# Performance work log

Hardware: AMD Instinct MI355X
Metric: run time of the kernel (lower is better)

Reference implementation:

```python
import jax, jax.numpy as jnp
import numpy as np

N = 50000
E = 800000
IN_CH = 128
HID = 64
HEADS = 4
EPS = 1e-5
NEG_SLOPE = 0.2


def _gat_conv(x, src, dst, W, a_src, a_dst, b, heads, out_ch, concat):
    n = x.shape[0]
    h = (x @ W).reshape(n, heads, out_ch)                      # [N,H,C]
    alpha_src = jnp.sum(h * a_src, axis=-1)                    # [N,H]
    alpha_dst = jnp.sum(h * a_dst, axis=-1)                    # [N,H]
    e = jax.nn.leaky_relu(alpha_src[src] + alpha_dst[dst], NEG_SLOPE)  # [E',H]
    # segment softmax over incoming edges of each destination node
    m = jax.ops.segment_max(e, dst, num_segments=n)            # [N,H]
    e = jnp.exp(e - m[dst])
    denom = jax.ops.segment_sum(e, dst, num_segments=n)        # [N,H]
    alpha = e / denom[dst]                                     # [E',H]
    msg = h[src] * alpha[:, :, None]                           # [E',H,C]
    out = jax.ops.segment_sum(msg, dst, num_segments=n)        # [N,H,C]
    if concat:
        out = out.reshape(n, heads * out_ch)
    else:
        out = out.mean(axis=1)
    return out + b


def _bn_eval(x, gamma, beta, mean, var):
    return (x - mean) * (gamma / jnp.sqrt(var + EPS)) + beta


def setup_inputs() -> dict:
    key = jax.random.key(0)
    ks = jax.random.split(key, 24)
    s = 0.1
    x = jax.random.normal(ks[0], (N, IN_CH), dtype=jnp.float32)
    edge_index = jax.random.randint(ks[1], (2, E), 0, N, dtype=jnp.int32)
    d0, d1 = IN_CH, HID * HEADS
    inp = {
        'x': x, 'edge_index': edge_index,
        # layer 0: in_ch -> hidden, heads=4, concat
        'W0': jax.random.normal(ks[2], (d0, HEADS * HID), jnp.float32) * s,
        'as0': jax.random.normal(ks[3], (HEADS, HID), jnp.float32) * s,
        'ad0': jax.random.normal(ks[4], (HEADS, HID), jnp.float32) * s,
        'b0': jax.random.normal(ks[5], (HEADS * HID,), jnp.float32) * s,
        # layer 1: hidden*heads -> hidden, heads=4, concat
        'W1': jax.random.normal(ks[6], (d1, HEADS * HID), jnp.float32) * s,
        'as1': jax.random.normal(ks[7], (HEADS, HID), jnp.float32) * s,
        'ad1': jax.random.normal(ks[8], (HEADS, HID), jnp.float32) * s,
        'b1': jax.random.normal(ks[9], (HEADS * HID,), jnp.float32) * s,
        # layer 2: hidden*heads -> 1, heads=1, no concat
        'W2': jax.random.normal(ks[10], (d1, 1), jnp.float32) * s,
        'as2': jax.random.normal(ks[11], (1, 1), jnp.float32) * s,
        'ad2': jax.random.normal(ks[12], (1, 1), jnp.float32) * s,
        'b2': jax.random.normal(ks[13], (1,), jnp.float32) * s,
        # batchnorm (eval) params for the two hidden layers
        'g0': jnp.ones((d1,), jnp.float32),
        'be0': jnp.zeros((d1,), jnp.float32),
        'm0': jax.random.normal(ks[14], (d1,), jnp.float32) * s,
        'v0': jnp.ones((d1,), jnp.float32),
        'g1': jnp.ones((d1,), jnp.float32),
        'be1': jnp.zeros((d1,), jnp.float32),
        'm1': jax.random.normal(ks[15], (d1,), jnp.float32) * s,
        'v1': jnp.ones((d1,), jnp.float32),
    }
    return inp


def reference(x, edge_index, W0, as0, ad0, b0, W1, as1, ad1, b1,
              W2, as2, ad2, b2, g0, be0, m0, v0, g1, be1, m1, v1):
    n = x.shape[0]
    loops = jnp.arange(n, dtype=edge_index.dtype)
    src = jnp.concatenate([edge_index[0], loops])  # add self-loops (PyG default)
    dst = jnp.concatenate([edge_index[1], loops])

    # layer 0 (no residual: shapes differ)
    h = _gat_conv(x, src, dst, W0, as0, ad0, b0, HEADS, HID, True)
    h = jax.nn.elu(_bn_eval(h, g0, be0, m0, v0))

    # layer 1 (residual: shapes match)
    res = h
    h = _gat_conv(h, src, dst, W1, as1, ad1, b1, HEADS, HID, True)
    h = jax.nn.elu(_bn_eval(h, g1, be1, m1, v1)) + res

    # output layer: heads=1, concat=False -> [N,1]
    out = _gat_conv(h, src, dst, W2, as2, ad2, b2, 1, 1, False)
    return out.squeeze(-1)
```

## Files before the change

kernel.cpp:

```cpp
#include <hip/hip_runtime.h>
#include <math.h>

#define NEG_SLOPE 0.2f
#define BN_EPS 1e-5f

typedef __attribute__((ext_vector_type(8))) short bf16x8;
typedef __attribute__((ext_vector_type(4))) float f32x4;

static __device__ __forceinline__ unsigned short f2bf(float f){
    unsigned u = __float_as_uint(f);
    u += 0x7FFFu + ((u >> 16) & 1u);
    return (unsigned short)(u >> 16);
}
static __device__ __forceinline__ float bf2f(unsigned short v){
    return __uint_as_float((unsigned)v << 16);
}

static __device__ __forceinline__ void gload_lds16(const void* g, void* l){
    __builtin_amdgcn_global_load_lds(
        (const __attribute__((address_space(1))) void*)g,
        (__attribute__((address_space(3))) void*)l, 16, 0, 0);
}

__global__ void conv_hilo_kernel(const float* __restrict__ x,
                                 unsigned short* __restrict__ hi,
                                 unsigned short* __restrict__ lo, int n4)
{
    int i = blockIdx.x * 256 + threadIdx.x;
    if (i >= n4) return;
    const float4 v = ((const float4*)x)[i];
    ushort4 h4, l4;
    h4.x = f2bf(v.x); l4.x = f2bf(v.x - bf2f(h4.x));
    h4.y = f2bf(v.y); l4.y = f2bf(v.y - bf2f(h4.y));
    h4.z = f2bf(v.z); l4.z = f2bf(v.z - bf2f(h4.z));
    h4.w = f2bf(v.w); l4.w = f2bf(v.w - bf2f(h4.w));
    ((ushort4*)hi)[i] = h4; ((ushort4*)lo)[i] = l4;
}

__global__ void repack_w_kernel(const float* __restrict__ W,
                                unsigned short* __restrict__ wbhi,
                                unsigned short* __restrict__ wblo)
{
    const int o = blockIdx.x * 256 + threadIdx.x;
    const int j = o & 7, ln = (o >> 3) & 63, ct = (o >> 9) & 15, kt = o >> 13;
    const int k = kt * 32 + 8 * (ln >> 4) + j;
    const int col = ct * 16 + (ln & 15);
    const float v = W[k * 256 + col];
    const unsigned short hb = f2bf(v);
    wbhi[o] = hb; wblo[o] = f2bf(v - bf2f(hb));
}

template<int K>
__global__ __launch_bounds__(256) void mfma_gemm_alpha(
    const unsigned short* __restrict__ xhi, const unsigned short* __restrict__ xlo,
    const unsigned short* __restrict__ wbhi, const unsigned short* __restrict__ wblo,
    const float* __restrict__ a_s, const float* __restrict__ a_d,
    unsigned short* __restrict__ hout,
    float* __restrict__ asrc, float* __restrict__ adst, int N)
{
    __shared__ unsigned short xa[8][512];
    __shared__ unsigned short wb[32][512];
    const int t = threadIdx.x, lane = t & 63, wid = t >> 6;
    const int n0 = blockIdx.x * 64;

    f32x4 acc[4][4];
#pragma unroll
    for (int rt = 0; rt < 4; ++rt)
#pragma unroll
        for (int q = 0; q < 4; ++q) acc[rt][q] = (f32x4){0.f, 0.f, 0.f, 0.f};

    for (int kt = 0; kt < K / 32; ++kt){
        __syncthreads();
#pragma unroll
        for (int ii = 0; ii < 2; ++ii){
            const int i = wid * 2 + ii;
            const int rt = i >> 1, plane = i & 1;
            int node = n0 + rt * 16 + (lane & 15);
            if (node > N - 1) node = N - 1;
            const unsigned short* src = (plane ? xlo : xhi)
                + (size_t)node * K + kt * 32 + 8 * (lane >> 4);
            gload_lds16(src, &xa[i][0]);
        }
#pragma unroll
        for (int ii = 0; ii < 8; ++ii){
            const int i = wid * 8 + ii;
            const int ct = i >> 1, plane = i & 1;
            const unsigned short* base = plane ? wblo : wbhi;
            gload_lds16(base + ((size_t)(kt * 16 + ct) * 64 + lane) * 8, &wb[i][0]);
        }
        __syncthreads();

        bf16x8 a[4][2];
#pragma unroll
        for (int rt = 0; rt < 4; ++rt)
#pragma unroll
            for (int pl = 0; pl < 2; ++pl)
                a[rt][pl] = *(const bf16x8*)&xa[rt * 2 + pl][lane * 8];

#pragma unroll
        for (int q = 0; q < 4; ++q){
            const int cti = wid * 4 + q;
            const bf16x8 bhi = *(const bf16x8*)&wb[cti * 2 + 0][lane * 8];
            const bf16x8 blo = *(const bf16x8*)&wb[cti * 2 + 1][lane * 8];
#pragma unroll
            for (int rt = 0; rt < 4; ++rt){
                acc[rt][q] = __builtin_amdgcn_mfma_f32_16x16x32_bf16(a[rt][0], bhi, acc[rt][q], 0, 0, 0);
                acc[rt][q] = __builtin_amdgcn_mfma_f32_16x16x32_bf16(a[rt][1], bhi, acc[rt][q], 0, 0, 0);
                acc[rt][q] = __builtin_amdgcn_mfma_f32_16x16x32_bf16(a[rt][0], blo, acc[rt][q], 0, 0, 0);
            }
        }
    }

    const int l15 = lane & 15, lg = lane >> 4;
    float avs[4], avd[4];
#pragma unroll
    for (int q = 0; q < 4; ++q){
        avs[q] = a_s[wid * 64 + q * 16 + l15];
        avd[q] = a_d[wid * 64 + q * 16 + l15];
    }
    float sp[4][4], dp[4][4];
#pragma unroll
    for (int rt = 0; rt < 4; ++rt){
#pragma unroll
        for (int reg = 0; reg < 4; ++reg){
            const int node = n0 + rt * 16 + lg * 4 + reg;
            float s = 0.f, d = 0.f;
            unsigned short hv[4];
#pragma unroll
            for (int q = 0; q < 4; ++q){
                const float v = acc[rt][q][reg];
                s = fmaf(v, avs[q], s); d = fmaf(v, avd[q], d);
                hv[q] = f2bf(v);
            }
            if (node < N){
#pragma unroll
                for (int q = 0; q < 4; ++q)
                    hout[(size_t)node * 256 + (wid * 4 + q) * 16 + l15] = hv[q];
            }
            sp[rt][reg] = s; dp[rt][reg] = d;
        }
    }
#pragma unroll
    for (int off = 1; off <= 8; off <<= 1){
#pragma unroll
        for (int rt = 0; rt < 4; ++rt)
#pragma unroll
            for (int reg = 0; reg < 4; ++reg){
                sp[rt][reg] += __shfl_xor(sp[rt][reg], off, 64);
                dp[rt][reg] += __shfl_xor(dp[rt][reg], off, 64);
            }
    }
    if (l15 == 0){
#pragma unroll
        for (int rt = 0; rt < 4; ++rt)
#pragma unroll
            for (int reg = 0; reg < 4; ++reg){
                const int node = n0 + rt * 16 + lg * 4 + reg;
                if (node < N){
                    asrc[(size_t)node * 4 + wid] = sp[rt][reg];
                    adst[(size_t)node * 4 + wid] = dp[rt][reg];
                }
            }
    }
}

__global__ void deg_init_kernel(int* __restrict__ deg, int N){
    int i = blockIdx.x * blockDim.x + threadIdx.x;
    if (i < N) deg[i] = 1;
}

__global__ void deg_hist_kernel(const int* __restrict__ ei, int E, int* __restrict__ deg){
    int e = blockIdx.x * blockDim.x + threadIdx.x;
    if (e < E) atomicAdd(&deg[ei[E + e]], 1);
}

__global__ __launch_bounds__(256) void part_sum_kernel(const int* __restrict__ deg,
                                                       int* __restrict__ bsum, int N)
{
    __shared__ int red[256];
    const int t = threadIdx.x;
    const int i0 = blockIdx.x * 1024 + t * 4;
    int s = 0;
    if (i0 + 3 < N){
        const int4 v = *(const int4*)&deg[i0];
        s = v.x + v.y + v.z + v.w;
    } else {
#pragma unroll
        for (int j = 0; j < 4; ++j) if (i0 + j < N) s += deg[i0 + j];
    }
    red[t] = s; __syncthreads();
    for (int off = 128; off >= 1; off >>= 1){
        if (t < off) red[t] += red[t + off];
        __syncthreads();
    }
    if (t == 0) bsum[blockIdx.x] = red[0];
}

__global__ __launch_bounds__(256) void scan_part_kernel(int* __restrict__ bsum, int nb,
                                                        int* __restrict__ row, int N)
{
    __shared__ int sh[256];
    const int t = threadIdx.x;
    const int v = (t < nb) ? bsum[t] : 0;
    sh[t] = v; __syncthreads();
    for (int off = 1; off < 256; off <<= 1){
        int u = (t >= off) ? sh[t - off] : 0;
        __syncthreads();
        sh[t] += u;
        __syncthreads();
    }
    if (t < nb) bsum[t] = sh[t] - v;
    if (t == nb - 1) row[N] = sh[t];
}

__global__ __launch_bounds__(256) void distribute_kernel(const int* __restrict__ deg,
    const int* __restrict__ bsum, int* __restrict__ row, int* __restrict__ cursor, int N)
{
    __shared__ int ts[256];
    const int t = threadIdx.x;
    const int i0 = blockIdx.x * 1024 + t * 4;
    int d[4]; int s = 0;
#pragma unroll
    for (int j = 0; j < 4; ++j){ d[j] = (i0 + j < N) ? deg[i0 + j] : 0; s += d[j]; }
    ts[t] = s; __syncthreads();
    for (int off = 1; off < 256; off <<= 1){
        int u = (t >= off) ? ts[t - off] : 0;
        __syncthreads();
        ts[t] += u;
        __syncthreads();
    }
    int base = bsum[blockIdx.x] + ts[t] - s;
#pragma unroll
    for (int j = 0; j < 4; ++j){
        if (i0 + j < N){ row[i0 + j] = base; cursor[i0 + j] = base; base += d[j]; }
    }
}

__global__ void scatter_kernel(const int* __restrict__ ei, int E, int N,
                               int* __restrict__ cursor, int* __restrict__ csr)
{
    int e = blockIdx.x * blockDim.x + threadIdx.x;
    if (e >= E + N) return;
    int s, d;
    if (e < E){ s = ei[e]; d = ei[E + e]; } else { s = d = e - E; }
    int pos = atomicAdd(&cursor[d], 1);
    csr[pos] = s;
}

#define DEG_CAP 128
__global__ __launch_bounds__(256) void agg4_kernel(
    const int* __restrict__ row, const int* __restrict__ csr,
    const float* __restrict__ asrc, const float* __restrict__ adst,
    const unsigned short* __restrict__ h,
    const float* __restrict__ b, const float* __restrict__ g,
    const float* __restrict__ be, const float* __restrict__ mean,
    const float* __restrict__ var,
    const unsigned short* __restrict__ reshi, const unsigned short* __restrict__ reslo,
    unsigned short* __restrict__ outhi, unsigned short* __restrict__ outlo, int N)
{
    __shared__ float plds[4][(DEG_CAP + 4) * 4];
    __shared__ int   slds[4][DEG_CAP + 4];
    const int wid = threadIdx.x >> 6, lane = threadIdx.x & 63;
    const int node = blockIdx.x * 4 + wid;
    if (node >= N) return;
    const int beg = row[node], end = row[node + 1], deg = end - beg;
    const int degc = deg < DEG_CAP ? deg : DEG_CAP;
    const int head = lane >> 4;

    const float4 ad = *(const float4*)&adst[(size_t)node * 4];

    float d0 = 0.f, d1 = 0.f, d2 = 0.f, d3 = 0.f;
    for (int i = lane; i < deg; i += 64){
        const int s = csr[beg + i];
        const float4 as = *(const float4*)&asrc[(size_t)s * 4];
        float v0 = as.x + ad.x, v1 = as.y + ad.y, v2 = as.z + ad.z, v3 = as.w + ad.w;
        v0 = v0 > 0.f ? v0 : NEG_SLOPE * v0;
        v1 = v1 > 0.f ? v1 : NEG_SLOPE * v1;
        v2 = v2 > 0.f ? v2 : NEG_SLOPE * v2;
        v3 = v3 > 0.f ? v3 : NEG_SLOPE * v3;
        const float p0 = __expf(v0), p1 = __expf(v1);
        const float p2 = __expf(v2), p3 = __expf(v3);
        d0 += p0; d1 += p1; d2 += p2; d3 += p3;
        if (i < DEG_CAP){
            *(float4*)&plds[wid][i * 4] = make_float4(p0, p1, p2, p3);
            slds[wid][i] = s << 9;
        }
    }
    if (lane < 4){
        const int slot = degc + lane;
        *(float4*)&plds[wid][slot * 4] = make_float4(0.f, 0.f, 0.f, 0.f);
        slds[wid][slot] = 0;
    }
    for (int off = 32; off >= 1; off >>= 1){
        d0 += __shfl_xor(d0, off, 64); d1 += __shfl_xor(d1, off, 64);
        d2 += __shfl_xor(d2, off, 64); d3 += __shfl_xor(d3, off, 64);
    }

    float a0 = 0.f, a1 = 0.f, a2 = 0.f, a3 = 0.f;
    {
        const char* hb = (const char*)h + lane * 8;
        const float* pb = &plds[wid][0];
        const int* sb = &slds[wid][0];
        ushort4 hA = *(const ushort4*)(hb + sb[0]);
        ushort4 hB = *(const ushort4*)(hb + sb[1]);
        for (int i = 0; i < degc; i += 2){
            const ushort4 hC = *(const ushort4*)(hb + sb[i + 2]);
            const ushort4 hD = *(const ushort4*)(hb + sb[i + 3]);
            const float pA = pb[i * 4 + head];
            const float pB = pb[(i + 1) * 4 + head];
            a0 = fmaf(pA, bf2f(hA.x), a0); a1 = fmaf(pA, bf2f(hA.y), a1);
            a2 = fmaf(pA, bf2f(hA.z), a2); a3 = fmaf(pA, bf2f(hA.w), a3);
            a0 = fmaf(pB, bf2f(hB.x), a0); a1 = fmaf(pB, bf2f(hB.y), a1);
            a2 = fmaf(pB, bf2f(hB.z), a2); a3 = fmaf(pB, bf2f(hB.w), a3);
            hA = hC; hB = hD;
        }
    }

    for (int jj = beg + DEG_CAP; jj < end; ++jj){
        const int s = csr[jj];
        const float4 as = *(const float4*)&asrc[(size_t)s * 4];
        float e0 = as.x + ad.x, e1 = as.y + ad.y, e2 = as.z + ad.z, e3 = as.w + ad.w;
        float eh = (head == 0) ? e0 : (head == 1) ? e1 : (head == 2) ? e2 : e3;
        eh = eh > 0.f ? eh : NEG_SLOPE * eh;
        const float p = __expf(eh);
        const ushort4 hv = *(const ushort4*)&h[(size_t)s * 256 + lane * 4];
        a0 = fmaf(p, bf2f(hv.x), a0); a1 = fmaf(p, bf2f(hv.y), a1);
        a2 = fmaf(p, bf2f(hv.z), a2); a3 = fmaf(p, bf2f(hv.w), a3);
    }

    const int l15 = lane & 15;
    const float dsel = (head == 0) ? d0 : (head == 1) ? d1 : (head == 2) ? d2 : d3;
    const float rdi = 1.f / dsel;
    const int c0 = head * 64 + 4 * l15;
    const float4 bv  = *(const float4*)&b[c0];
    const float4 gv  = *(const float4*)&g[c0];
    const float4 bev = *(const float4*)&be[c0];
    const float4 mv  = *(const float4*)&mean[c0];
    const float4 vv4 = *(const float4*)&var[c0];
    const float ava[4]  = {a0, a1, a2, a3};
    const float bva[4]  = {bv.x, bv.y, bv.z, bv.w};
    const float gva[4]  = {gv.x, gv.y, gv.z, gv.w};
    const float beva[4] = {bev.x, bev.y, bev.z, bev.w};
    const float mva[4]  = {mv.x, mv.y, mv.z, mv.w};
    const float vva[4]  = {vv4.x, vv4.y, vv4.z, vv4.w};
    float rh[4] = {0.f, 0.f, 0.f, 0.f};
    if (reshi){
        const ushort4 r1 = *(const ushort4*)&reshi[(size_t)node * 256 + c0];
        const ushort4 r2 = *(const ushort4*)&reslo[(size_t)node * 256 + c0];
        rh[0] = bf2f(r1.x) + bf2f(r2.x); rh[1] = bf2f(r1.y) + bf2f(r2.y);
        rh[2] = bf2f(r1.z) + bf2f(r2.z); rh[3] = bf2f(r1.w) + bf2f(r2.w);
    }
    unsigned short hos[4], los[4];
#pragma unroll
    for (int j = 0; j < 4; ++j){
        float vvv = ava[j] * rdi + bva[j];
        vvv = (vvv - mva[j]) * (gva[j] * rsqrtf(vva[j] + BN_EPS)) + beva[j];
        vvv = vvv > 0.f ? vvv : (__expf(vvv) - 1.f);
        vvv += rh[j];
        const unsigned short hb2 = f2bf(vvv);
        hos[j] = hb2; los[j] = f2bf(vvv - bf2f(hb2));
    }
    ushort4 ho, lo4;
    ho.x = hos[0];  ho.y = hos[1];  ho.z = hos[2];  ho.w = hos[3];
    lo4.x = los[0]; lo4.y = los[1]; lo4.z = los[2]; lo4.w = los[3];
    *(ushort4*)&outhi[(size_t)node * 256 + c0] = ho;
    *(ushort4*)&outlo[(size_t)node * 256 + c0] = lo4;
}

__global__ __launch_bounds__(256) void gemm2_kernel(
    const unsigned short* __restrict__ xhi, const unsigned short* __restrict__ xlo,
    const float* __restrict__ W2, float* __restrict__ h2, int N)
{
    const int wid = threadIdx.x >> 6, lane = threadIdx.x & 63;
    const int n = blockIdx.x * 4 + wid;
    if (n >= N) return;
    float sum = 0.f;
#pragma unroll
    for (int i = 0; i < 4; ++i){
        const int c = i * 64 + lane;
        sum += (bf2f(xhi[(size_t)n * 256 + c]) + bf2f(xlo[(size_t)n * 256 + c])) * W2[c];
    }
    for (int off = 32; off >= 1; off >>= 1) sum += __shfl_xor(sum, off, 64);
    if (lane == 0) h2[n] = sum;
}

__global__ void agg2_kernel(const int* __restrict__ row, const int* __restrict__ csr,
                            const float* __restrict__ h2,
                            const float* __restrict__ as2, const float* __restrict__ ad2,
                            const float* __restrict__ b2, float* __restrict__ out, int N)
{
    const int n = blockIdx.x * blockDim.x + threadIdx.x;
    if (n >= N) return;
    const float A_s = as2[0];
    const float hd  = h2[n] * ad2[0];
    const int beg = row[n], end = row[n + 1];
    float den = 0.f, acc = 0.f;
    for (int i = beg; i < end; ++i){
        const float hv = h2[csr[i]];
        float a = fmaf(A_s, hv, hd);
        a = a > 0.f ? a : NEG_SLOPE * a;
        const float p = __expf(a);
        den += p; acc = fmaf(p, hv, acc);
    }
    out[n] = acc / den + b2[0];
}

extern "C" void kernel_launch(void* const* d_in, const int* in_sizes, int n_in,
                              void* d_out, int out_size, void* d_ws, size_t ws_size,
                              hipStream_t stream)
{
    const float* x   = (const float*)d_in[0];
    const int*   ei  = (const int*)  d_in[1];
    const float* W0  = (const float*)d_in[2];
    const float* as0 = (const float*)d_in[3];
    const float* ad0 = (const float*)d_in[4];
    const float* b0  = (const float*)d_in[5];
    const float* W1  = (const float*)d_in[6];
    const float* as1 = (const float*)d_in[7];
    const float* ad1 = (const float*)d_in[8];
    const float* b1  = (const float*)d_in[9];
    const float* W2  = (const float*)d_in[10];
    const float* as2 = (const float*)d_in[11];
    const float* ad2 = (const float*)d_in[12];
    const float* b2  = (const float*)d_in[13];
    const float* g0  = (const float*)d_in[14];
    const float* be0 = (const float*)d_in[15];
    const float* m0  = (const float*)d_in[16];
    const float* v0  = (const float*)d_in[17];
    const float* g1  = (const float*)d_in[18];
    const float* be1 = (const float*)d_in[19];
    const float* m1  = (const float*)d_in[20];
    const float* v1  = (const float*)d_in[21];

    const int N = in_sizes[0] / 128;
    const int E = in_sizes[1] / 2;
    const int EN = E + N;

    char* w = (char*)d_ws;
    unsigned short* H    = (unsigned short*)w;  w += (size_t)N * 256 * 2;
    unsigned short* X0hi = (unsigned short*)w;
    unsigned short* X0lo = X0hi + (size_t)N * 128;
    unsigned short* P1hi = X0hi;
    w += (size_t)N * 256 * 2;
    unsigned short* P0hi = (unsigned short*)w;  w += (size_t)N * 256 * 2;
    unsigned short* P0lo = (unsigned short*)w;  w += (size_t)N * 256 * 2;
    unsigned short* P1lo = (unsigned short*)w;  w += (size_t)N * 256 * 2;
    float*    asrc   = (float*)w;   w += (size_t)N * 4 * 4;
    float*    adst   = (float*)w;   w += (size_t)N * 4 * 4;
    int*      deg    = (int*)w;     w += (size_t)N * 4;
    int*      cursor = (int*)w;     w += (size_t)N * 4;
    int*      csr    = (int*)w;     w += (size_t)EN * 4;
    float*    h2     = (float*)w;   w += (size_t)N * 4;
    int*      bsum   = (int*)w;     w += 1024;
    unsigned short* Wb0hi = (unsigned short*)w; w += (size_t)128 * 256 * 2;
    unsigned short* Wb0lo = (unsigned short*)w; w += (size_t)128 * 256 * 2;
    unsigned short* Wb1hi = (unsigned short*)w; w += (size_t)256 * 256 * 2;
    unsigned short* Wb1lo = (unsigned short*)w; w += (size_t)256 * 256 * 2;
    int*      rowp   = (int*)w;     w += (size_t)(N + 1) * 4;

    const int gN64  = (N + 63) / 64;
    const int gN4   = (N + 3) / 4;
    const int gNt   = (N + 255) / 256;
    const int gE    = (E + 255) / 256;
    const int gEN   = (EN + 255) / 256;
    const int nb    = (N + 1023) / 1024;

    conv_hilo_kernel<<<(N * 128 / 4 + 255) / 256, 256, 0, stream>>>(x, X0hi, X0lo, N * 128 / 4);
    repack_w_kernel<<<128, 256, 0, stream>>>(W0, Wb0hi, Wb0lo);
    repack_w_kernel<<<256, 256, 0, stream>>>(W1, Wb1hi, Wb1lo);
    deg_init_kernel<<<gNt, 256, 0, stream>>>(deg, N);
    deg_hist_kernel<<<gE, 256, 0, stream>>>(ei, E, deg);
    part_sum_kernel<<<nb, 256, 0, stream>>>(deg, bsum, N);
    scan_part_kernel<<<1, 256, 0, stream>>>(bsum, nb, rowp, N);
    distribute_kernel<<<nb, 256, 0, stream>>>(deg, bsum, rowp, cursor, N);
    scatter_kernel<<<gEN, 256, 0, stream>>>(ei, E, N, cursor, csr);

    mfma_gemm_alpha<128><<<gN64, 256, 0, stream>>>(X0hi, X0lo, Wb0hi, Wb0lo,
                                                   as0, ad0, H, asrc, adst, N);
    agg4_kernel<<<gN4, 256, 0, stream>>>(rowp, csr, asrc, adst, H,
                                         b0, g0, be0, m0, v0,
                                         nullptr, nullptr, P0hi, P0lo, N);

    mfma_gemm_alpha<256><<<gN64, 256, 0, stream>>>(P0hi, P0lo, Wb1hi, Wb1lo,
                                                   as1, ad1, H, asrc, adst, N);
    agg4_kernel<<<gN4, 256, 0, stream>>>(rowp, csr, asrc, adst, H,
                                         b1, g1, be1, m1, v1,
                                         P0hi, P0lo, P1hi, P1lo, N);

    gemm2_kernel<<<gN4, 256, 0, stream>>>(P1hi, P1lo, W2, h2, N);
    agg2_kernel<<<gNt, 256, 0, stream>>>(rowp, csr, h2, as2, ad2, b2, (float*)d_out, N);
}
```

Baseline: 346.0 us.

## Fuse hi/lo split into GEMM, fold layer-2 GEMV into aggregation, merge prep kernels

```diff
diff --git a/kernel.cpp b/kernel.cpp
--- a/kernel.cpp
+++ b/kernel.cpp
@@ -22,43 +22,43 @@
         (__attribute__((address_space(3))) void*)l, 16, 0, 0);
 }
 
-__global__ void conv_hilo_kernel(const float* __restrict__ x,
-                                 unsigned short* __restrict__ hi,
-                                 unsigned short* __restrict__ lo, int n4)
-{
-    int i = blockIdx.x * 256 + threadIdx.x;
-    if (i >= n4) return;
-    const float4 v = ((const float4*)x)[i];
-    ushort4 h4, l4;
-    h4.x = f2bf(v.x); l4.x = f2bf(v.x - bf2f(h4.x));
-    h4.y = f2bf(v.y); l4.y = f2bf(v.y - bf2f(h4.y));
-    h4.z = f2bf(v.z); l4.z = f2bf(v.z - bf2f(h4.z));
-    h4.w = f2bf(v.w); l4.w = f2bf(v.w - bf2f(h4.w));
-    ((ushort4*)hi)[i] = h4; ((ushort4*)lo)[i] = l4;
-}
-
-__global__ void repack_w_kernel(const float* __restrict__ W,
-                                unsigned short* __restrict__ wbhi,
-                                unsigned short* __restrict__ wblo)
-{
-    const int o = blockIdx.x * 256 + threadIdx.x;
+static __device__ __forceinline__ void repack_one(const float* __restrict__ W,
+    unsigned short* __restrict__ whi, unsigned short* __restrict__ wlo, int o)
+{
     const int j = o & 7, ln = (o >> 3) & 63, ct = (o >> 9) & 15, kt = o >> 13;
     const int k = kt * 32 + 8 * (ln >> 4) + j;
     const int col = ct * 16 + (ln & 15);
     const float v = W[k * 256 + col];
     const unsigned short hb = f2bf(v);
-    wbhi[o] = hb; wblo[o] = f2bf(v - bf2f(hb));
+    whi[o] = hb; wlo[o] = f2bf(v - bf2f(hb));
+}
+
+__global__ void prep_kernel(const float* __restrict__ W0,
+    unsigned short* __restrict__ w0hi, unsigned short* __restrict__ w0lo,
+    const float* __restrict__ W1,
+    unsigned short* __restrict__ w1hi, unsigned short* __restrict__ w1lo,
+    int* __restrict__ deg, int N)
+{
+    const int bid = blockIdx.x, t = threadIdx.x;
+    if (bid < 128){
+        repack_one(W0, w0hi, w0lo, bid * 256 + t);
+    } else if (bid < 384){
+        repack_one(W1, w1hi, w1lo, (bid - 128) * 256 + t);
+    } else {
+        const int i = (bid - 384) * 256 + t;
+        if (i < N) deg[i] = 1;
+    }
 }
 
 template<int K>
 __global__ __launch_bounds__(256) void mfma_gemm_alpha(
-    const unsigned short* __restrict__ xhi, const unsigned short* __restrict__ xlo,
+    const float* __restrict__ x,
     const unsigned short* __restrict__ wbhi, const unsigned short* __restrict__ wblo,
     const float* __restrict__ a_s, const float* __restrict__ a_d,
     unsigned short* __restrict__ hout,
     float* __restrict__ asrc, float* __restrict__ adst, int N)
 {
-    __shared__ unsigned short xa[8][512];
+    __shared__ float xaf[4][2][64][4];
     __shared__ unsigned short wb[32][512];
     const int t = threadIdx.x, lane = t & 63, wid = t >> 6;
     const int n0 = blockIdx.x * 64;
@@ -74,12 +74,11 @@
 #pragma unroll
         for (int ii = 0; ii < 2; ++ii){
             const int i = wid * 2 + ii;
-            const int rt = i >> 1, plane = i & 1;
+            const int rt = i >> 1, half = i & 1;
             int node = n0 + rt * 16 + (lane & 15);
             if (node > N - 1) node = N - 1;
-            const unsigned short* src = (plane ? xlo : xhi)
-                + (size_t)node * K + kt * 32 + 8 * (lane >> 4);
-            gload_lds16(src, &xa[i][0]);
+            const float* src = &x[(size_t)node * K + kt * 32 + 8 * (lane >> 4) + half * 4];
+            gload_lds16(src, &xaf[rt][half][0][0]);
         }
 #pragma unroll
         for (int ii = 0; ii < 8; ++ii){
@@ -90,12 +89,19 @@
         }
         __syncthreads();
 
-        bf16x8 a[4][2];
-#pragma unroll
-        for (int rt = 0; rt < 4; ++rt)
-#pragma unroll
-            for (int pl = 0; pl < 2; ++pl)
-                a[rt][pl] = *(const bf16x8*)&xa[rt * 2 + pl][lane * 8];
+        bf16x8 ahi[4], alo[4];
+#pragma unroll
+        for (int rt = 0; rt < 4; ++rt){
+            const float4 f0 = *(const float4*)&xaf[rt][0][lane][0];
+            const float4 f1 = *(const float4*)&xaf[rt][1][lane][0];
+            const float fv[8] = {f0.x, f0.y, f0.z, f0.w, f1.x, f1.y, f1.z, f1.w};
+#pragma unroll
+            for (int j = 0; j < 8; ++j){
+                const unsigned short hb = f2bf(fv[j]);
+                ahi[rt][j] = (short)hb;
+                alo[rt][j] = (short)f2bf(fv[j] - bf2f(hb));
+            }
+        }
 
 #pragma unroll
         for (int q = 0; q < 4; ++q){
@@ -104,9 +110,9 @@
             const bf16x8 blo = *(const bf16x8*)&wb[cti * 2 + 1][lane * 8];
 #pragma unroll
             for (int rt = 0; rt < 4; ++rt){
-                acc[rt][q] = __builtin_amdgcn_mfma_f32_16x16x32_bf16(a[rt][0], bhi, acc[rt][q], 0, 0, 0);
-                acc[rt][q] = __builtin_amdgcn_mfma_f32_16x16x32_bf16(a[rt][1], bhi, acc[rt][q], 0, 0, 0);
-                acc[rt][q] = __builtin_amdgcn_mfma_f32_16x16x32_bf16(a[rt][0], blo, acc[rt][q], 0, 0, 0);
+                acc[rt][q] = __builtin_amdgcn_mfma_f32_16x16x32_bf16(ahi[rt], bhi, acc[rt][q], 0, 0, 0);
+                acc[rt][q] = __builtin_amdgcn_mfma_f32_16x16x32_bf16(alo[rt], bhi, acc[rt][q], 0, 0, 0);
+                acc[rt][q] = __builtin_amdgcn_mfma_f32_16x16x32_bf16(ahi[rt], blo, acc[rt][q], 0, 0, 0);
             }
         }
     }
@@ -162,11 +168,6 @@
                 }
             }
     }
-}
-
-__global__ void deg_init_kernel(int* __restrict__ deg, int N){
-    int i = blockIdx.x * blockDim.x + threadIdx.x;
-    if (i < N) deg[i] = 1;
 }
 
 __global__ void deg_hist_kernel(const int* __restrict__ ei, int E, int* __restrict__ deg){
@@ -248,6 +249,7 @@
 }
 
 #define DEG_CAP 128
+template<bool LAST>
 __global__ __launch_bounds__(256) void agg4_kernel(
     const int* __restrict__ row, const int* __restrict__ csr,
     const float* __restrict__ asrc, const float* __restrict__ adst,
@@ -255,11 +257,13 @@
     const float* __restrict__ b, const float* __restrict__ g,
     const float* __restrict__ be, const float* __restrict__ mean,
     const float* __restrict__ var,
-    const unsigned short* __restrict__ reshi, const unsigned short* __restrict__ reslo,
-    unsigned short* __restrict__ outhi, unsigned short* __restrict__ outlo, int N)
-{
-    __shared__ float plds[4][(DEG_CAP + 4) * 4];
-    __shared__ int   slds[4][DEG_CAP + 4];
+    const float* __restrict__ res,
+    float* __restrict__ outp,
+    const float* __restrict__ W2,
+    int N)
+{
+    __shared__ float plds[4][DEG_CAP * 4];
+    __shared__ int   slds[4][DEG_CAP];
     const int wid = threadIdx.x >> 6, lane = threadIdx.x & 63;
     const int node = blockIdx.x * 4 + wid;
     if (node >= N) return;
@@ -286,11 +290,6 @@
             slds[wid][i] = s << 9;
         }
     }
-    if (lane < 4){
-        const int slot = degc + lane;
-        *(float4*)&plds[wid][slot * 4] = make_float4(0.f, 0.f, 0.f, 0.f);
-        slds[wid][slot] = 0;
-    }
     for (int off = 32; off >= 1; off >>= 1){
         d0 += __shfl_xor(d0, off, 64); d1 += __shfl_xor(d1, off, 64);
         d2 += __shfl_xor(d2, off, 64); d3 += __shfl_xor(d3, off, 64);
@@ -301,19 +300,20 @@
         const char* hb = (const char*)h + lane * 8;
         const float* pb = &plds[wid][0];
         const int* sb = &slds[wid][0];
-        ushort4 hA = *(const ushort4*)(hb + sb[0]);
-        ushort4 hB = *(const ushort4*)(hb + sb[1]);
-        for (int i = 0; i < degc; i += 2){
-            const ushort4 hC = *(const ushort4*)(hb + sb[i + 2]);
-            const ushort4 hD = *(const ushort4*)(hb + sb[i + 3]);
-            const float pA = pb[i * 4 + head];
-            const float pB = pb[(i + 1) * 4 + head];
-            a0 = fmaf(pA, bf2f(hA.x), a0); a1 = fmaf(pA, bf2f(hA.y), a1);
-            a2 = fmaf(pA, bf2f(hA.z), a2); a3 = fmaf(pA, bf2f(hA.w), a3);
-            a0 = fmaf(pB, bf2f(hB.x), a0); a1 = fmaf(pB, bf2f(hB.y), a1);
-            a2 = fmaf(pB, bf2f(hB.z), a2); a3 = fmaf(pB, bf2f(hB.w), a3);
-            hA = hC; hB = hD;
-        }
+#define EDGE_BODY(slot)                                                        \
+        {                                                                      \
+            const float p_ = pb[(slot) * 4 + head];                            \
+            const ushort4 hv_ = *(const ushort4*)(hb + sb[slot]);              \
+            a0 = fmaf(p_, bf2f(hv_.x), a0); a1 = fmaf(p_, bf2f(hv_.y), a1);    \
+            a2 = fmaf(p_, bf2f(hv_.z), a2); a3 = fmaf(p_, bf2f(hv_.w), a3);    \
+        }
+        int i = 0;
+        for (; i + 2 <= degc; i += 2){
+            EDGE_BODY(i);
+            EDGE_BODY(i + 1);
+        }
+        for (; i < degc; ++i) EDGE_BODY(i);
+#undef EDGE_BODY
     }
 
     for (int jj = beg + DEG_CAP; jj < end; ++jj){
@@ -344,44 +344,27 @@
     const float mva[4]  = {mv.x, mv.y, mv.z, mv.w};
     const float vva[4]  = {vv4.x, vv4.y, vv4.z, vv4.w};
     float rh[4] = {0.f, 0.f, 0.f, 0.f};
-    if (reshi){
-        const ushort4 r1 = *(const ushort4*)&reshi[(size_t)node * 256 + c0];
-        const ushort4 r2 = *(const ushort4*)&reslo[(size_t)node * 256 + c0];
-        rh[0] = bf2f(r1.x) + bf2f(r2.x); rh[1] = bf2f(r1.y) + bf2f(r2.y);
-        rh[2] = bf2f(r1.z) + bf2f(r2.z); rh[3] = bf2f(r1.w) + bf2f(r2.w);
-    }
-    unsigned short hos[4], los[4];
+    if (LAST){
+        const float4 rv = *(const float4*)&res[(size_t)node * 256 + c0];
+        rh[0] = rv.x; rh[1] = rv.y; rh[2] = rv.z; rh[3] = rv.w;
+    }
+    float vvv[4];
 #pragma unroll
     for (int j = 0; j < 4; ++j){
-        float vvv = ava[j] * rdi + bva[j];
-        vvv = (vvv - mva[j]) * (gva[j] * rsqrtf(vva[j] + BN_EPS)) + beva[j];
-        vvv = vvv > 0.f ? vvv : (__expf(vvv) - 1.f);
-        vvv += rh[j];
-        const unsigned short hb2 = f2bf(vvv);
-        hos[j] = hb2; los[j] = f2bf(vvv - bf2f(hb2));
-    }
-    ushort4 ho, lo4;
-    ho.x = hos[0];  ho.y = hos[1];  ho.z = hos[2];  ho.w = hos[3];
-    lo4.x = los[0]; lo4.y = los[1]; lo4.z = los[2]; lo4.w = los[3];
-    *(ushort4*)&outhi[(size_t)node * 256 + c0] = ho;
-    *(ushort4*)&outlo[(size_t)node * 256 + c0] = lo4;
-}
-
-__global__ __launch_bounds__(256) void gemm2_kernel(
-    const unsigned short* __restrict__ xhi, const unsigned short* __restrict__ xlo,
-    const float* __restrict__ W2, float* __restrict__ h2, int N)
-{
-    const int wid = threadIdx.x >> 6, lane = threadIdx.x & 63;
-    const int n = blockIdx.x * 4 + wid;
-    if (n >= N) return;
-    float sum = 0.f;
-#pragma unroll
-    for (int i = 0; i < 4; ++i){
-        const int c = i * 64 + lane;
-        sum += (bf2f(xhi[(size_t)n * 256 + c]) + bf2f(xlo[(size_t)n * 256 + c])) * W2[c];
-    }
-    for (int off = 32; off >= 1; off >>= 1) sum += __shfl_xor(sum, off, 64);
-    if (lane == 0) h2[n] = sum;
+        float v = ava[j] * rdi + bva[j];
+        v = (v - mva[j]) * (gva[j] * rsqrtf(vva[j] + BN_EPS)) + beva[j];
+        v = v > 0.f ? v : (__expf(v) - 1.f);
+        vvv[j] = v + rh[j];
+    }
+    if (!LAST){
+        *(float4*)&outp[(size_t)node * 256 + c0] =
+            make_float4(vvv[0], vvv[1], vvv[2], vvv[3]);
+    } else {
+        const float4 w2v = *(const float4*)&W2[c0];
+        float part = vvv[0] * w2v.x + vvv[1] * w2v.y + vvv[2] * w2v.z + vvv[3] * w2v.w;
+        for (int off = 32; off >= 1; off >>= 1) part += __shfl_xor(part, off, 64);
+        if (lane == 0) outp[node] = part;
+    }
 }
 
 __global__ void agg2_kernel(const int* __restrict__ row, const int* __restrict__ csr,
@@ -437,14 +420,8 @@
     const int EN = E + N;
 
     char* w = (char*)d_ws;
-    unsigned short* H    = (unsigned short*)w;  w += (size_t)N * 256 * 2;
-    unsigned short* X0hi = (unsigned short*)w;
-    unsigned short* X0lo = X0hi + (size_t)N * 128;
-    unsigned short* P1hi = X0hi;
-    w += (size_t)N * 256 * 2;
-    unsigned short* P0hi = (unsigned short*)w;  w += (size_t)N * 256 * 2;
-    unsigned short* P0lo = (unsigned short*)w;  w += (size_t)N * 256 * 2;
-    unsigned short* P1lo = (unsigned short*)w;  w += (size_t)N * 256 * 2;
+    unsigned short* H  = (unsigned short*)w;  w += (size_t)N * 256 * 2;
+    float*    P0     = (float*)w;   w += (size_t)N * 256 * 4;
     float*    asrc   = (float*)w;   w += (size_t)N * 4 * 4;
     float*    adst   = (float*)w;   w += (size_t)N * 4 * 4;
     int*      deg    = (int*)w;     w += (size_t)N * 4;
@@ -465,28 +442,24 @@
     const int gEN   = (EN + 255) / 256;
     const int nb    = (N + 1023) / 1024;
 
-    conv_hilo_kernel<<<(N * 128 / 4 + 255) / 256, 256, 0, stream>>>(x, X0hi, X0lo, N * 128 / 4);
-    repack_w_kernel<<<128, 256, 0, stream>>>(W0, Wb0hi, Wb0lo);
-    repack_w_kernel<<<256, 256, 0, stream>>>(W1, Wb1hi, Wb1lo);
-    deg_init_kernel<<<gNt, 256, 0, stream>>>(deg, N);
+    prep_kernel<<<384 + gNt, 256, 0, stream>>>(W0, Wb0hi, Wb0lo, W1, Wb1hi, Wb1lo, deg, N);
     deg_hist_kernel<<<gE, 256, 0, stream>>>(ei, E, deg);
     part_sum_kernel<<<nb, 256, 0, stream>>>(deg, bsum, N);
     scan_part_kernel<<<1, 256, 0, stream>>>(bsum, nb, rowp, N);
     distribute_kernel<<<nb, 256, 0, stream>>>(deg, bsum, rowp, cursor, N);
     scatter_kernel<<<gEN, 256, 0, stream>>>(ei, E, N, cursor, csr);
 
-    mfma_gemm_alpha<128><<<gN64, 256, 0, stream>>>(X0hi, X0lo, Wb0hi, Wb0lo,
+    mfma_gemm_alpha<128><<<gN64, 256, 0, stream>>>(x, Wb0hi, Wb0lo,
                                                    as0, ad0, H, asrc, adst, N);
-    agg4_kernel<<<gN4, 256, 0, stream>>>(rowp, csr, asrc, adst, H,
-                                         b0, g0, be0, m0, v0,
-                                         nullptr, nullptr, P0hi, P0lo, N);
-
-    mfma_gemm_alpha<256><<<gN64, 256, 0, stream>>>(P0hi, P0lo, Wb1hi, Wb1lo,
+    agg4_kernel<false><<<gN4, 256, 0, stream>>>(rowp, csr, asrc, adst, H,
+                                                b0, g0, be0, m0, v0,
+                                                nullptr, P0, nullptr, N);
+
+    mfma_gemm_alpha<256><<<gN64, 256, 0, stream>>>(P0, Wb1hi, Wb1lo,
                                                    as1, ad1, H, asrc, adst, N);
-    agg4_kernel<<<gN4, 256, 0, stream>>>(rowp, csr, asrc, adst, H,
-                                         b1, g1, be1, m1, v1,
-                                         P0hi, P0lo, P1hi, P1lo, N);
-
-    gemm2_kernel<<<gN4, 256, 0, stream>>>(P1hi, P1lo, W2, h2, N);
+    agg4_kernel<true><<<gN4, 256, 0, stream>>>(rowp, csr, asrc, adst, H,
+                                               b1, g1, be1, m1, v1,
+                                               P0, h2, W2, N);
+
     agg2_kernel<<<gNt, 256, 0, stream>>>(rowp, csr, h2, as2, ad2, b2, (float*)d_out, N);
 }
```

Measured after the change: 331.5 us. -4.2%, faster.
